# Kernel tuning notes

Hardware: AMD Instinct MI355X
Metric: run time of the kernel (lower is better)

Reference implementation:

```python
import jax, jax.numpy as jnp
import numpy as np

HEADS = 8
DIM_HEAD = 64
SCALE = DIM_HEAD ** -0.5


def setup_inputs() -> dict:
    key = jax.random.key(0)
    ks = jax.random.split(key, 8)
    B, Nq, Dq = 4, 2048, 512
    Nk, Dc = 1024, 768
    inner = HEADS * DIM_HEAD  # 512
    x = jax.random.normal(ks[0], (B, Nq, Dq), dtype=jnp.float32)
    context = jax.random.normal(ks[1], (B, Nk, Dc), dtype=jnp.float32)
    # Linear weights stored [in, out]; y = x @ W (+ b)
    Wq = jax.random.normal(ks[2], (Dq, inner), dtype=jnp.float32) / np.sqrt(Dq)
    Wk = jax.random.normal(ks[3], (Dc, inner), dtype=jnp.float32) / np.sqrt(Dc)
    Wv = jax.random.normal(ks[4], (Dc, inner), dtype=jnp.float32) / np.sqrt(Dc)
    Wo = jax.random.normal(ks[5], (inner, Dq), dtype=jnp.float32) / np.sqrt(inner)
    bo = jax.random.normal(ks[6], (Dq,), dtype=jnp.float32) * 0.01
    return {"x": x, "context": context, "Wq": Wq, "Wk": Wk, "Wv": Wv, "Wo": Wo, "bo": bo}


def reference(x, context, Wq, Wk, Wv, Wo, bo):
    B, Nq, _ = x.shape
    Nk = context.shape[1]
    # projections
    q = x @ Wq          # [B, Nq, h*d]
    k = context @ Wk    # [B, Nk, h*d]
    v = context @ Wv    # [B, Nk, h*d]
    # split heads: b n (h d) -> b h n d
    q = q.reshape(B, Nq, HEADS, DIM_HEAD).transpose(0, 2, 1, 3)
    k = k.reshape(B, Nk, HEADS, DIM_HEAD).transpose(0, 2, 1, 3)
    v = v.reshape(B, Nk, HEADS, DIM_HEAD).transpose(0, 2, 1, 3)
    # fp32 QK^T (ATTN_PRECISION == 'fp32' path)
    sim = jnp.einsum('bhid,bhjd->bhij', q.astype(jnp.float32), k.astype(jnp.float32)) * SCALE
    attn = jax.nn.softmax(sim, axis=-1)
    out = jnp.einsum('bhij,bhjd->bhid', attn, v)  # [B, h, Nq, d]
    out = out.transpose(0, 2, 1, 3).reshape(B, Nq, HEADS * DIM_HEAD)
    return out @ Wo + bo  # dropout=0 -> identity
```

## Files before the change

kernel.cpp:

```cpp
#include <hip/hip_runtime.h>
#include <cstddef>
#include <cstdint>

typedef __attribute__((ext_vector_type(8))) short bf16x8;
typedef __attribute__((ext_vector_type(4))) float f32x4;

static __device__ __forceinline__ short f2bf(float f) {
    union { float f; unsigned u; } x;
    x.f = f;
    unsigned r = (x.u + 0x7FFFu + ((x.u >> 16) & 1u)) >> 16;
    return (short)r;
}

typedef __attribute__((address_space(3))) unsigned lds_u;
typedef const __attribute__((address_space(1))) unsigned glb_u;
static __device__ __forceinline__ void gld_lds16(const void* g, void* l) {
    __builtin_amdgcn_global_load_lds((glb_u*)g, (lds_u*)l, 16, 0, 0);
}

__global__ __launch_bounds__(256) void prep_kernel(
    const float* __restrict__ x, const float* __restrict__ c,
    short* __restrict__ xb, short* __restrict__ cb,
    const float* __restrict__ Wq, const float* __restrict__ Wk,
    const float* __restrict__ Wv, const float* __restrict__ Wo,
    short* __restrict__ wqT, short* __restrict__ wkvT, short* __restrict__ woT)
{
    __shared__ float T[32][33];
    const int bid = blockIdx.x;
    const int tid = threadIdx.x;
    if (bid < 7168) {
        int i = bid * 256 + tid;
        const float* src; short* dst; int off;
        if (i < 1048576) { src = x; dst = xb; off = i; }
        else { src = c; dst = cb; off = i - 1048576; }
        float4 v = ((const float4*)src)[off];
        ushort4 w;
        w.x = (unsigned short)f2bf(v.x); w.y = (unsigned short)f2bf(v.y);
        w.z = (unsigned short)f2bf(v.z); w.w = (unsigned short)f2bf(v.w);
        ((ushort4*)dst)[off] = w;
        return;
    }
    const int w0 = bid - 7168;
    const int z = w0 / 384, rem = w0 % 384;
    const int yt = rem >> 4, xt = rem & 15;
    const float* src; short* dst; int R;
    if (z == 0)      { src = Wq; dst = wqT;  R = 512; }
    else if (z == 1) { src = Wk; dst = wkvT; R = 768; }
    else if (z == 2) { src = Wv; dst = wkvT + (size_t)512 * 768; R = 768; }
    else             { src = Wo; dst = woT;  R = 512; }
    if (yt * 32 >= R) return;
    {
        int r = tid >> 3, c4 = (tid & 7) * 4;
        float4 v = *(const float4*)&src[(size_t)(yt * 32 + r) * 512 + xt * 32 + c4];
        T[r][c4] = v.x; T[r][c4 + 1] = v.y; T[r][c4 + 2] = v.z; T[r][c4 + 3] = v.w;
    }
    __syncthreads();
    {
        int cc = tid >> 3, r4 = (tid & 7) * 4;
        ushort4 w;
        w.x = (unsigned short)f2bf(T[r4][cc]);     w.y = (unsigned short)f2bf(T[r4 + 1][cc]);
        w.z = (unsigned short)f2bf(T[r4 + 2][cc]); w.w = (unsigned short)f2bf(T[r4 + 3][cc]);
        *(ushort4*)&dst[(size_t)(xt * 32 + cc) * R + yt * 32 + r4] = w;
    }
}

__global__ __launch_bounds__(256) void vtrans_kernel(
    const short* __restrict__ v, short* __restrict__ vT)
{
    __shared__ short T[32][33];
    const int b = blockIdx.z, yt = blockIdx.y, xt = blockIdx.x;
    const int tid = threadIdx.x;
    {
        int r = tid >> 3, c4 = (tid & 7) * 4;
        ushort4 vv = *(const ushort4*)&v[((size_t)(b * 1024 + yt * 32 + r)) * 1024 + xt * 32 + c4];
        T[r][c4] = (short)vv.x; T[r][c4 + 1] = (short)vv.y;
        T[r][c4 + 2] = (short)vv.z; T[r][c4 + 3] = (short)vv.w;
    }
    __syncthreads();
    {
        int cc = tid >> 3, r4 = (tid & 7) * 4;
        ushort4 w;
        w.x = (unsigned short)T[r4][cc];     w.y = (unsigned short)T[r4 + 1][cc];
        w.z = (unsigned short)T[r4 + 2][cc]; w.w = (unsigned short)T[r4 + 3][cc];
        int kk = yt * 32 + r4;
        int kl = kk & 63;
        int g  = ((kl >> 5) << 2) | ((kl >> 2) & 3);
        int p  = (kk & ~63) | (g << 3) | (((kl >> 4) & 1) << 2);
        *(ushort4*)&vT[((size_t)(b * 512 + xt * 32 + cc)) * 1024 + p] = w;
    }
}

static __device__ __forceinline__ void gemm_core(
    const short* __restrict__ A, const short* __restrict__ BT, int K,
    int bm, int bn, short* As, short* Bs, f32x4 acc[4][4])
{
    const int tid  = threadIdx.x;
    const int lane = tid & 63;
    const int wave = tid >> 6;
    const int lm   = lane & 15;
    const int quad = lane >> 4;
    const int wm = (wave >> 1) * 64;
    const int wn = (wave & 1) * 64;
    const int c = tid >> 7, r = tid & 127;

    const short* Ag = &A[(size_t)(bm + r) * K + c * 8];
    const short* Bg = &BT[(size_t)(bn + r) * K + c * 8];

    gld_lds16(Ag,      &As[tid * 8]);
    gld_lds16(Ag + 16, &As[(tid + 256) * 8]);
    gld_lds16(Bg,      &Bs[tid * 8]);
    gld_lds16(Bg + 16, &Bs[(tid + 256) * 8]);
    Ag += 32; Bg += 32;
    gld_lds16(Ag,      &As[4096 + tid * 8]);
    gld_lds16(Ag + 16, &As[4096 + (tid + 256) * 8]);
    gld_lds16(Bg,      &Bs[4096 + tid * 8]);
    gld_lds16(Bg + 16, &Bs[4096 + (tid + 256) * 8]);
    Ag += 32; Bg += 32;

    const int NT = K >> 5;
    int ocur = 0;
    int onxt = 2 * 4096;
    for (int t = 0; t < NT; ++t) {
        if (t < NT - 1) asm volatile("s_waitcnt vmcnt(4)" ::: "memory");
        else            asm volatile("s_waitcnt vmcnt(0)" ::: "memory");
        __builtin_amdgcn_s_barrier();
        __builtin_amdgcn_sched_barrier(0);
        if (t < NT - 2) {
            gld_lds16(Ag,      &As[onxt + tid * 8]);
            gld_lds16(Ag + 16, &As[onxt + (tid + 256) * 8]);
            gld_lds16(Bg,      &Bs[onxt + tid * 8]);
            gld_lds16(Bg + 16, &Bs[onxt + (tid + 256) * 8]);
            Ag += 32; Bg += 32;
        }
        const short* Ac = As + ocur;
        const short* Bc = Bs + ocur;
        bf16x8 af[4], bfr[4];
        #pragma unroll
        for (int i = 0; i < 4; ++i)
            af[i] = *(const bf16x8*)&Ac[(quad * 128 + wm + i * 16 + lm) * 8];
        #pragma unroll
        for (int j = 0; j < 4; ++j)
            bfr[j] = *(const bf16x8*)&Bc[(quad * 128 + wn + j * 16 + lm) * 8];
        __builtin_amdgcn_s_setprio(1);
        #pragma unroll
        for (int i = 0; i < 4; ++i)
            #pragma unroll
            for (int j = 0; j < 4; ++j)
                acc[i][j] = __builtin_amdgcn_mfma_f32_16x16x32_bf16(
                    af[i], bfr[j], acc[i][j], 0, 0, 0);
        __builtin_amdgcn_s_setprio(0);
        ocur += 4096; if (ocur == 12288) ocur = 0;
        onxt += 4096; if (onxt == 12288) onxt = 0;
    }
}

__global__ __launch_bounds__(256) void qkv_kernel(
    const short* __restrict__ xb, const short* __restrict__ cb,
    const short* __restrict__ wqT, const short* __restrict__ wkvT,
    short* __restrict__ qb, short* __restrict__ kvb)
{
    __shared__ short As[3 * 4096];
    __shared__ short Bs[3 * 4096];
    const int L = (blockIdx.x & 7) * 64 + (blockIdx.x >> 3);
    const short *A, *BT; short* C; int K, ldc, bm, bn; float cscale;
    if (L < 256) { A = xb; BT = wqT;  C = qb;  K = 512; ldc = 512;
                   bm = (L >> 2) * 128; bn = (L & 3) * 128;
                   cscale = 0.18033688f; }
    else { int b2 = L - 256; A = cb; BT = wkvT; C = kvb; K = 768; ldc = 1024;
           bm = (b2 >> 3) * 128; bn = (b2 & 7) * 128; cscale = 1.0f; }

    f32x4 acc[4][4] = {};
    gemm_core(A, BT, K, bm, bn, As, Bs, acc);

    const int lane = threadIdx.x & 63, wave = threadIdx.x >> 6;
    const int lm = lane & 15, quad = lane >> 4;
    const int wm = (wave >> 1) * 64, wn = (wave & 1) * 64;
    #pragma unroll
    for (int j = 0; j < 4; ++j) {
        int col = bn + wn + j * 16 + lm;
        #pragma unroll
        for (int i = 0; i < 4; ++i) {
            int row0 = bm + wm + i * 16 + quad * 4;
            #pragma unroll
            for (int r = 0; r < 4; ++r)
                C[(size_t)(row0 + r) * ldc + col] = f2bf(acc[i][j][r] * cscale);
        }
    }
}

__global__ __launch_bounds__(256) void ogemm_kernel(
    const short* __restrict__ ob, const short* __restrict__ woT,
    const float* __restrict__ bias, float* __restrict__ out)
{
    __shared__ short As[3 * 4096];
    __shared__ short Bs[3 * 4096];
    const int L = (blockIdx.x & 7) * 32 + (blockIdx.x >> 3);
    const int bm = (L >> 2) * 128, bn = (L & 3) * 128;

    f32x4 acc[4][4] = {};
    gemm_core(ob, woT, 512, bm, bn, As, Bs, acc);

    const int lane = threadIdx.x & 63, wave = threadIdx.x >> 6;
    const int lm = lane & 15, quad = lane >> 4;
    const int wm = (wave >> 1) * 64, wn = (wave & 1) * 64;
    #pragma unroll
    for (int j = 0; j < 4; ++j) {
        int col = bn + wn + j * 16 + lm;
        float bv = bias[col];
        #pragma unroll
        for (int i = 0; i < 4; ++i) {
            int row0 = bm + wm + i * 16 + quad * 4;
            #pragma unroll
            for (int r = 0; r < 4; ++r)
                out[(size_t)(row0 + r) * 512 + col] = acc[i][j][r] + bv;
        }
    }
}

__global__ __launch_bounds__(256) void attn_kernel(
    const short* __restrict__ q, const short* __restrict__ k,
    const short* __restrict__ vT, short* __restrict__ o)
{
    __shared__ short Ks[3 * 4096];
    __shared__ short Vs[3 * 4096];

    const int tid  = threadIdx.x;
    const int lane = tid & 63;
    const int wave = tid >> 6;
    const int lm   = lane & 15;
    const int quad = lane >> 4;

    const int bid = blockIdx.x;
    const int xcdq = bid >> 3;
    const int hb = (bid & 7) + ((xcdq >> 4) << 3);
    const int qt = xcdq & 15;
    const int h = hb & 7, b = hb >> 3;

    const size_t qrow0 = (size_t)b * 2048 + qt * 128;
    const size_t krow0 = (size_t)b * 1024;
    const int hcol = h * 64;
    const size_t vrow0 = ((size_t)b * 8 + h) * 64;

    const short* kg = &k[(krow0 + (tid & 63)) * 1024 + hcol + (tid >> 6) * 8];
    const short* vg = &vT[(vrow0 + (tid & 63)) * 1024 + (tid >> 6) * 8];

    const short* qrow0p = &q[(qrow0 + wave * 32 + lm) * 512 + hcol];
    const short* qrow1p = qrow0p + 16 * 512;
    bf16x8 qf00 = *(const bf16x8*)&qrow0p[quad * 8];
    bf16x8 qf01 = *(const bf16x8*)&qrow0p[32 + quad * 8];
    bf16x8 qf10 = *(const bf16x8*)&qrow1p[quad * 8];
    bf16x8 qf11 = *(const bf16x8*)&qrow1p[32 + quad * 8];
    asm volatile("" :: "v"(qf00), "v"(qf01), "v"(qf10), "v"(qf11));

    gld_lds16(kg,      &Ks[tid * 8]);
    gld_lds16(kg + 32, &Ks[(tid + 256) * 8]);
    gld_lds16(vg,      &Vs[tid * 8]);
    gld_lds16(vg + 32, &Vs[(tid + 256) * 8]);
    kg += 64 * 1024; vg += 64;
    gld_lds16(kg,      &Ks[4096 + tid * 8]);
    gld_lds16(kg + 32, &Ks[4096 + (tid + 256) * 8]);
    gld_lds16(vg,      &Vs[4096 + tid * 8]);
    gld_lds16(vg + 32, &Vs[4096 + (tid + 256) * 8]);
    kg += 64 * 1024; vg += 64;

    f32x4 oacc[2][4] = {};
    float lsum[2] = {0.0f, 0.0f};
    const int fro = (quad * 64 + lm) * 8;

    int ocur = 0;
    int onxt = 2 * 4096;
    for (int t = 0; t < 16; ++t) {
        if (t < 15) asm volatile("s_waitcnt vmcnt(4)" ::: "memory");
        else        asm volatile("s_waitcnt vmcnt(0)" ::: "memory");
        __builtin_amdgcn_s_barrier();
        __builtin_amdgcn_sched_barrier(0);
        if (t < 14) {
            gld_lds16(kg,      &Ks[onxt + tid * 8]);
            gld_lds16(kg + 32, &Ks[onxt + (tid + 256) * 8]);
            gld_lds16(vg,      &Vs[onxt + tid * 8]);
            gld_lds16(vg + 32, &Vs[onxt + (tid + 256) * 8]);
            kg += 64 * 1024; vg += 64;
        }
        const short* Kc = &Ks[ocur + fro];
        const short* Vc = &Vs[ocur + fro];

        f32x4 sacc0[4] = {}, sacc1[4] = {};
        __builtin_amdgcn_s_setprio(1);
        #pragma unroll
        for (int j = 0; j < 4; ++j) {
            bf16x8 kf0 = *(const bf16x8*)&Kc[(j * 16) * 8];
            bf16x8 kf1 = *(const bf16x8*)&Kc[(256 + j * 16) * 8];
            sacc0[j] = __builtin_amdgcn_mfma_f32_16x16x32_bf16(kf0, qf00, sacc0[j], 0, 0, 0);
            sacc1[j] = __builtin_amdgcn_mfma_f32_16x16x32_bf16(kf0, qf10, sacc1[j], 0, 0, 0);
            sacc0[j] = __builtin_amdgcn_mfma_f32_16x16x32_bf16(kf1, qf01, sacc0[j], 0, 0, 0);
            sacc1[j] = __builtin_amdgcn_mfma_f32_16x16x32_bf16(kf1, qf11, sacc1[j], 0, 0, 0);
        }
        __builtin_amdgcn_s_setprio(0);

        union { unsigned u[4]; bf16x8 v; } pf00, pf01, pf10, pf11;
        #pragma unroll
        for (int j = 0; j < 4; ++j) {
            #pragma unroll
            for (int rp = 0; rp < 2; ++rp) {
                float a0 = __builtin_amdgcn_exp2f(sacc0[j][2 * rp]);
                float a1 = __builtin_amdgcn_exp2f(sacc0[j][2 * rp + 1]);
                float b0 = __builtin_amdgcn_exp2f(sacc1[j][2 * rp]);
                float b1 = __builtin_amdgcn_exp2f(sacc1[j][2 * rp + 1]);
                lsum[0] += a0 + a1;
                lsum[1] += b0 + b1;
                unsigned pa, pb;
                asm("v_cvt_pk_bf16_f32 %0, %1, %2" : "=v"(pa) : "v"(a0), "v"(a1));
                asm("v_cvt_pk_bf16_f32 %0, %1, %2" : "=v"(pb) : "v"(b0), "v"(b1));
                if (j < 2) { pf00.u[j * 2 + rp] = pa; pf10.u[j * 2 + rp] = pb; }
                else       { pf01.u[(j - 2) * 2 + rp] = pa; pf11.u[(j - 2) * 2 + rp] = pb; }
            }
        }

        __builtin_amdgcn_s_setprio(1);
        #pragma unroll
        for (int j = 0; j < 4; ++j) {
            bf16x8 vf0 = *(const bf16x8*)&Vc[(j * 16) * 8];
            bf16x8 vf1 = *(const bf16x8*)&Vc[(256 + j * 16) * 8];
            oacc[0][j] = __builtin_amdgcn_mfma_f32_16x16x32_bf16(pf00.v, vf0, oacc[0][j], 0, 0, 0);
            oacc[1][j] = __builtin_amdgcn_mfma_f32_16x16x32_bf16(pf10.v, vf0, oacc[1][j], 0, 0, 0);
            oacc[0][j] = __builtin_amdgcn_mfma_f32_16x16x32_bf16(pf01.v, vf1, oacc[0][j], 0, 0, 0);
            oacc[1][j] = __builtin_amdgcn_mfma_f32_16x16x32_bf16(pf11.v, vf1, oacc[1][j], 0, 0, 0);
        }
        __builtin_amdgcn_s_setprio(0);

        ocur += 4096; if (ocur == 12288) ocur = 0;
        onxt += 4096; if (onxt == 12288) onxt = 0;
    }

    #pragma unroll
    for (int g = 0; g < 2; ++g) {
        float s = lsum[g];
        s += __shfl_xor(s, 16);
        s += __shfl_xor(s, 32);
        const float inv = 1.0f / s;
        float invr[4];
        #pragma unroll
        for (int r = 0; r < 4; ++r)
            invr[r] = __shfl(inv, quad * 20 + r);
        #pragma unroll
        for (int j = 0; j < 4; ++j) {
            int col = hcol + j * 16 + lm;
            #pragma unroll
            for (int r = 0; r < 4; ++r) {
                size_t row = qrow0 + wave * 32 + g * 16 + quad * 4 + r;
                o[row * 512 + col] = f2bf(oacc[g][j][r] * invr[r]);
            }
        }
    }
}

extern "C" void kernel_launch(void* const* d_in, const int* in_sizes, int n_in,
                              void* d_out, int out_size, void* d_ws, size_t ws_size,
                              hipStream_t stream)
{
    const float* x   = (const float*)d_in[0];
    const float* ctx = (const float*)d_in[1];
    const float* Wq  = (const float*)d_in[2];
    const float* Wk  = (const float*)d_in[3];
    const float* Wv  = (const float*)d_in[4];
    const float* Wo  = (const float*)d_in[5];
    const float* bo  = (const float*)d_in[6];

    char* ws = (char*)d_ws;
    short* xb   = (short*)(ws);
    short* cb   = (short*)(ws + (8u << 20));
    short* wqT  = (short*)(ws + (14u << 20));
    short* wkvT = (short*)(ws + (14u << 20) + (512u << 10));
    short* woT  = (short*)(ws + (16u << 20));
    short* qb   = (short*)(ws + (16u << 20) + (512u << 10));
    short* kvb  = (short*)(ws + (24u << 20) + (512u << 10));
    short* ob   = xb;
    short* vT   = cb;

    prep_kernel<<<8704, 256, 0, stream>>>(x, ctx, xb, cb, Wq, Wk, Wv, Wo, wqT, wkvT, woT);
    qkv_kernel<<<512, 256, 0, stream>>>(xb, cb, wqT, wkvT, qb, kvb);
    vtrans_kernel<<<dim3(16, 32, 4), 256, 0, stream>>>(kvb + 512, vT);
    attn_kernel<<<512, 256, 0, stream>>>(qb, kvb, vT, ob);
    ogemm_kernel<<<256, 256, 0, stream>>>(ob, woT, bo, (float*)d_out);
}
```

Measured before the change: 172.5 us.

## Use 128-key tiles with double buffering in attention kernel

The attention kernel now processes 128 keys per iteration instead of 64, and replaces the 3-stage 64-key LDS ring with a 2-stage 128-key double buffer. This halves the number of barriers and loop iterations and gives each iteration more MFMA work to hide LDS loads. In exchange it holds more score registers and waits for vmcnt(0) each iteration, which removes one stage of prefetch depth. LDS use grows from 48 KB to 64 KB per block, which may reduce occupancy.

```diff
diff --git a/kernel.cpp b/kernel.cpp
--- a/kernel.cpp
+++ b/kernel.cpp
@@ -221,8 +221,8 @@
     const short* __restrict__ q, const short* __restrict__ k,
     const short* __restrict__ vT, short* __restrict__ o)
 {
-    __shared__ short Ks[3 * 4096];
-    __shared__ short Vs[3 * 4096];
+    __shared__ short Ks[2 * 8192];
+    __shared__ short Vs[2 * 8192];
 
     const int tid  = threadIdx.x;
     const int lane = tid & 63;
@@ -241,8 +241,18 @@
     const int hcol = h * 64;
     const size_t vrow0 = ((size_t)b * 8 + h) * 64;
 
-    const short* kg = &k[(krow0 + (tid & 63)) * 1024 + hcol + (tid >> 6) * 8];
-    const short* vg = &vT[(vrow0 + (tid & 63)) * 1024 + (tid >> 6) * 8];
+    const int rk = tid & 127, ck = tid >> 7;
+    const int dv = tid & 63,  nv = tid >> 6;
+    const short* kg = &k[(krow0 + rk) * 1024 + hcol + ck * 8];
+    const short* vg = &vT[(vrow0 + dv) * 1024 + nv * 8];
+
+    #pragma unroll
+    for (int c = 0; c < 4; ++c)
+        gld_lds16(kg + c * 16, &Ks[((ck + 2 * c) * 128 + rk) * 8]);
+    #pragma unroll
+    for (int c = 0; c < 4; ++c)
+        gld_lds16(vg + c * 32, &Vs[((nv + 4 * c) * 64 + dv) * 8]);
+    kg += 128 * 1024; vg += 128;
 
     const short* qrow0p = &q[(qrow0 + wave * 32 + lm) * 512 + hcol];
     const short* qrow1p = qrow0p + 16 * 512;
@@ -252,84 +262,74 @@
     bf16x8 qf11 = *(const bf16x8*)&qrow1p[32 + quad * 8];
     asm volatile("" :: "v"(qf00), "v"(qf01), "v"(qf10), "v"(qf11));
 
-    gld_lds16(kg,      &Ks[tid * 8]);
-    gld_lds16(kg + 32, &Ks[(tid + 256) * 8]);
-    gld_lds16(vg,      &Vs[tid * 8]);
-    gld_lds16(vg + 32, &Vs[(tid + 256) * 8]);
-    kg += 64 * 1024; vg += 64;
-    gld_lds16(kg,      &Ks[4096 + tid * 8]);
-    gld_lds16(kg + 32, &Ks[4096 + (tid + 256) * 8]);
-    gld_lds16(vg,      &Vs[4096 + tid * 8]);
-    gld_lds16(vg + 32, &Vs[4096 + (tid + 256) * 8]);
-    kg += 64 * 1024; vg += 64;
-
     f32x4 oacc[2][4] = {};
     float lsum[2] = {0.0f, 0.0f};
-    const int fro = (quad * 64 + lm) * 8;
-
-    int ocur = 0;
-    int onxt = 2 * 4096;
-    for (int t = 0; t < 16; ++t) {
-        if (t < 15) asm volatile("s_waitcnt vmcnt(4)" ::: "memory");
-        else        asm volatile("s_waitcnt vmcnt(0)" ::: "memory");
+    const int frk = (quad * 128 + lm) * 8;
+    const int frv = (quad * 64 + lm) * 8;
+
+    for (int t = 0; t < 8; ++t) {
+        asm volatile("s_waitcnt vmcnt(0)" ::: "memory");
         __builtin_amdgcn_s_barrier();
         __builtin_amdgcn_sched_barrier(0);
-        if (t < 14) {
-            gld_lds16(kg,      &Ks[onxt + tid * 8]);
-            gld_lds16(kg + 32, &Ks[onxt + (tid + 256) * 8]);
-            gld_lds16(vg,      &Vs[onxt + tid * 8]);
-            gld_lds16(vg + 32, &Vs[onxt + (tid + 256) * 8]);
-            kg += 64 * 1024; vg += 64;
-        }
-        const short* Kc = &Ks[ocur + fro];
-        const short* Vc = &Vs[ocur + fro];
-
-        f32x4 sacc0[4] = {}, sacc1[4] = {};
+        const short* Kc = &Ks[(t & 1) * 8192];
+        const short* Vc = &Vs[(t & 1) * 8192];
+        if (t < 7) {
+            short* Kn = &Ks[((t & 1) ^ 1) * 8192];
+            short* Vn = &Vs[((t & 1) ^ 1) * 8192];
+            #pragma unroll
+            for (int c = 0; c < 4; ++c)
+                gld_lds16(kg + c * 16, &Kn[((ck + 2 * c) * 128 + rk) * 8]);
+            #pragma unroll
+            for (int c = 0; c < 4; ++c)
+                gld_lds16(vg + c * 32, &Vn[((nv + 4 * c) * 64 + dv) * 8]);
+            kg += 128 * 1024; vg += 128;
+        }
+
+        f32x4 s0[8], s1[8];
+        #pragma unroll
+        for (int j = 0; j < 8; ++j) { s0[j] = (f32x4){}; s1[j] = (f32x4){}; }
         __builtin_amdgcn_s_setprio(1);
         #pragma unroll
-        for (int j = 0; j < 4; ++j) {
-            bf16x8 kf0 = *(const bf16x8*)&Kc[(j * 16) * 8];
-            bf16x8 kf1 = *(const bf16x8*)&Kc[(256 + j * 16) * 8];
-            sacc0[j] = __builtin_amdgcn_mfma_f32_16x16x32_bf16(kf0, qf00, sacc0[j], 0, 0, 0);
-            sacc1[j] = __builtin_amdgcn_mfma_f32_16x16x32_bf16(kf0, qf10, sacc1[j], 0, 0, 0);
-            sacc0[j] = __builtin_amdgcn_mfma_f32_16x16x32_bf16(kf1, qf01, sacc0[j], 0, 0, 0);
-            sacc1[j] = __builtin_amdgcn_mfma_f32_16x16x32_bf16(kf1, qf11, sacc1[j], 0, 0, 0);
+        for (int j = 0; j < 8; ++j) {
+            bf16x8 kf0 = *(const bf16x8*)&Kc[frk + j * 128];
+            bf16x8 kf1 = *(const bf16x8*)&Kc[frk + 4096 + j * 128];
+            s0[j] = __builtin_amdgcn_mfma_f32_16x16x32_bf16(kf0, qf00, s0[j], 0, 0, 0);
+            s1[j] = __builtin_amdgcn_mfma_f32_16x16x32_bf16(kf0, qf10, s1[j], 0, 0, 0);
+            s0[j] = __builtin_amdgcn_mfma_f32_16x16x32_bf16(kf1, qf01, s0[j], 0, 0, 0);
+            s1[j] = __builtin_amdgcn_mfma_f32_16x16x32_bf16(kf1, qf11, s1[j], 0, 0, 0);
         }
         __builtin_amdgcn_s_setprio(0);
 
-        union { unsigned u[4]; bf16x8 v; } pf00, pf01, pf10, pf11;
-        #pragma unroll
-        for (int j = 0; j < 4; ++j) {
+        union { unsigned u[4]; bf16x8 v; } pf0[4], pf1[4];
+        #pragma unroll
+        for (int j = 0; j < 8; ++j) {
             #pragma unroll
             for (int rp = 0; rp < 2; ++rp) {
-                float a0 = __builtin_amdgcn_exp2f(sacc0[j][2 * rp]);
-                float a1 = __builtin_amdgcn_exp2f(sacc0[j][2 * rp + 1]);
-                float b0 = __builtin_amdgcn_exp2f(sacc1[j][2 * rp]);
-                float b1 = __builtin_amdgcn_exp2f(sacc1[j][2 * rp + 1]);
+                float a0 = __builtin_amdgcn_exp2f(s0[j][2 * rp]);
+                float a1 = __builtin_amdgcn_exp2f(s0[j][2 * rp + 1]);
+                float b0 = __builtin_amdgcn_exp2f(s1[j][2 * rp]);
+                float b1 = __builtin_amdgcn_exp2f(s1[j][2 * rp + 1]);
                 lsum[0] += a0 + a1;
                 lsum[1] += b0 + b1;
                 unsigned pa, pb;
                 asm("v_cvt_pk_bf16_f32 %0, %1, %2" : "=v"(pa) : "v"(a0), "v"(a1));
                 asm("v_cvt_pk_bf16_f32 %0, %1, %2" : "=v"(pb) : "v"(b0), "v"(b1));
-                if (j < 2) { pf00.u[j * 2 + rp] = pa; pf10.u[j * 2 + rp] = pb; }
-                else       { pf01.u[(j - 2) * 2 + rp] = pa; pf11.u[(j - 2) * 2 + rp] = pb; }
+                pf0[j >> 1].u[(j & 1) * 2 + rp] = pa;
+                pf1[j >> 1].u[(j & 1) * 2 + rp] = pb;
             }
         }
 
         __builtin_amdgcn_s_setprio(1);
         #pragma unroll
-        for (int j = 0; j < 4; ++j) {
-            bf16x8 vf0 = *(const bf16x8*)&Vc[(j * 16) * 8];
-            bf16x8 vf1 = *(const bf16x8*)&Vc[(256 + j * 16) * 8];
-            oacc[0][j] = __builtin_amdgcn_mfma_f32_16x16x32_bf16(pf00.v, vf0, oacc[0][j], 0, 0, 0);
-            oacc[1][j] = __builtin_amdgcn_mfma_f32_16x16x32_bf16(pf10.v, vf0, oacc[1][j], 0, 0, 0);
-            oacc[0][j] = __builtin_amdgcn_mfma_f32_16x16x32_bf16(pf01.v, vf1, oacc[0][j], 0, 0, 0);
-            oacc[1][j] = __builtin_amdgcn_mfma_f32_16x16x32_bf16(pf11.v, vf1, oacc[1][j], 0, 0, 0);
+        for (int jd = 0; jd < 4; ++jd) {
+            #pragma unroll
+            for (int s = 0; s < 4; ++s) {
+                bf16x8 vf = *(const bf16x8*)&Vc[frv + s * 2048 + jd * 128];
+                oacc[0][jd] = __builtin_amdgcn_mfma_f32_16x16x32_bf16(pf0[s].v, vf, oacc[0][jd], 0, 0, 0);
+                oacc[1][jd] = __builtin_amdgcn_mfma_f32_16x16x32_bf16(pf1[s].v, vf, oacc[1][jd], 0, 0, 0);
+            }
         }
         __builtin_amdgcn_s_setprio(0);
-
-        ocur += 4096; if (ocur == 12288) ocur = 0;
-        onxt += 4096; if (onxt == 12288) onxt = 0;
     }
 
     #pragma unroll
```

Result: no change. 171.9 us (-0.4%).
